# Optimization experiments

Measured on AMD Instinct MI355X. Metric: run time of the kernel, lower is better.

The kernel has to match this reference:

```python
import jax, jax.numpy as jnp
import numpy as np

C = 256
NUM_HEADS = 8
GROUPS = 8
EPS = 1e-5


def setup_inputs() -> dict:
    key = jax.random.key(0)
    ks = jax.random.split(key, 7)
    B, H, W = 2, 64, 64
    x = jax.random.normal(ks[0], (B, C, H, W), dtype=jnp.float32)
    gn_weight = jnp.ones((C,), dtype=jnp.float32)
    gn_bias = jnp.zeros((C,), dtype=jnp.float32)
    # 1x1 convs == per-pixel linear layers
    w_qkv = jax.random.normal(ks[1], (3 * C, C), dtype=jnp.float32) * (1.0 / np.sqrt(C))
    b_qkv = jax.random.normal(ks[2], (3 * C,), dtype=jnp.float32) * 0.01
    w_proj = jax.random.normal(ks[3], (C, C), dtype=jnp.float32) * (1.0 / np.sqrt(C))
    b_proj = jax.random.normal(ks[4], (C,), dtype=jnp.float32) * 0.01
    return {"x": x, "gn_weight": gn_weight, "gn_bias": gn_bias,
            "w_qkv": w_qkv, "b_qkv": b_qkv, "w_proj": w_proj, "b_proj": b_proj}


def reference(x, gn_weight, gn_bias, w_qkv, b_qkv, w_proj, b_proj):
    B, Cc, H, W = x.shape
    nh = NUM_HEADS
    hd = Cc // nh
    N = H * W
    scale = hd ** (-0.5)

    # GroupNorm(8, C): normalize over (C/G, H, W) per group, biased variance
    xg = x.reshape(B, GROUPS, Cc // GROUPS, H, W)
    mean = xg.mean(axis=(2, 3, 4), keepdims=True)
    var = xg.var(axis=(2, 3, 4), keepdims=True)
    hn = (xg - mean) * jax.lax.rsqrt(var + EPS)
    hn = hn.reshape(B, Cc, H, W) * gn_weight[None, :, None, None] + gn_bias[None, :, None, None]

    hf = hn.reshape(B, Cc, N)                       # [B, C, N]
    qkv = jnp.einsum('oc,bcn->bon', w_qkv, hf) + b_qkv[None, :, None]  # [B, 3C, N]
    qkv = qkv.reshape(B, 3, nh, hd, N)
    # q,k,v: [B, nh, N, hd]
    q = jnp.transpose(qkv[:, 0], (0, 1, 3, 2))
    k = jnp.transpose(qkv[:, 1], (0, 1, 3, 2))
    v = jnp.transpose(qkv[:, 2], (0, 1, 3, 2))

    attn = jnp.einsum('bhqd,bhkd->bhqk', q, k) * scale  # [B, nh, N, N]
    attn = jax.nn.softmax(attn, axis=-1)
    o = jnp.einsum('bhqk,bhkd->bhqd', attn, v)           # [B, nh, N, hd]
    o = jnp.transpose(o, (0, 1, 3, 2)).reshape(B, Cc, H, W)

    of = o.reshape(B, Cc, N)
    out = jnp.einsum('oc,bcn->bon', w_proj, of) + b_proj[None, :, None]
    return out.reshape(B, Cc, H, W)
```

## Files before the change

### kernel.cpp

```cpp
#include <hip/hip_runtime.h>


typedef _Float16 half8 __attribute__((ext_vector_type(8)));
typedef __fp16   fp16x2 __attribute__((ext_vector_type(2)));
typedef float    f32x4 __attribute__((ext_vector_type(4)));
typedef int      int2v __attribute__((ext_vector_type(2)));
typedef int      int4v __attribute__((ext_vector_type(4)));

__device__ __forceinline__ f32x4 mfma16(half8 a, half8 b, f32x4 c) {
  return __builtin_amdgcn_mfma_f32_16x16x32_f16(a, b, c, 0, 0, 0);
}

#if __has_builtin(__builtin_amdgcn_exp2f)
#define EXP2(x) __builtin_amdgcn_exp2f(x)
#else
#define EXP2(x) exp2f(x)
#endif

__device__ __forceinline__ unsigned short h_bits(_Float16 h) {
  return __builtin_bit_cast(unsigned short, h);
}
__device__ __forceinline__ int h2_bits(fp16x2 h) {
  return __builtin_bit_cast(int, h);
}

constexpr float CSCALE = (float)(1.4426950408889634 / 5.656854249492381);

__global__ __launch_bounds__(256) void gn_stats(const float* __restrict__ x,
                                                float* __restrict__ stats) {
  const int bg = blockIdx.x, ch = blockIdx.y, tid = threadIdx.x;
  const float* p = x + (size_t)bg * 131072 + (size_t)ch * 4096;
  float s = 0.f, ss = 0.f;
#pragma unroll
  for (int j = 0; j < 4; ++j) {
    f32x4 v = *(const f32x4*)(p + j * 1024 + tid * 4);
#pragma unroll
    for (int k = 0; k < 4; ++k) { s += v[k]; ss += v[k] * v[k]; }
  }
#pragma unroll
  for (int m = 1; m <= 32; m <<= 1) { s += __shfl_xor(s, m); ss += __shfl_xor(ss, m); }
  __shared__ float red[8];
  const int wv = tid >> 6;
  if ((tid & 63) == 0) { red[wv * 2] = s; red[wv * 2 + 1] = ss; }
  __syncthreads();
  if (tid == 0) {
    float S = red[0] + red[2] + red[4] + red[6];
    float SS = red[1] + red[3] + red[5] + red[7];
    atomicAdd(&stats[bg * 2], S);
    atomicAdd(&stats[bg * 2 + 1], SS);
  }
}

__global__ __launch_bounds__(256) void gn_apply(const float* __restrict__ x,
                                                const float* __restrict__ gw,
                                                const float* __restrict__ gb,
                                                const float* __restrict__ stats,
                                                _Float16* __restrict__ hn) {
  __shared__ float tile[64 * 65];
  const int tid = threadIdx.x;
  const int a = tid & 15;
  const int row16 = tid >> 4;
  const int b = blockIdx.z, c0 = blockIdx.y * 64, n0 = blockIdx.x * 64;
#pragma unroll
  for (int m = 0; m < 4; ++m) {
    const int cl = row16 + 16 * m;
    const int c = c0 + cl;
    const int g = c >> 5;
    const float s = stats[(b * 8 + g) * 2];
    const float ss = stats[(b * 8 + g) * 2 + 1];
    const float mean = s * (1.f / 131072.f);
    const float var = ss * (1.f / 131072.f) - mean * mean;
    const float rstd = rsqrtf(var + 1e-5f);
    const float ga = gw[c] * rstd;
    const float be = gb[c] - mean * ga;
    f32x4 xv = *(const f32x4*)(x + ((size_t)(b * 256 + c)) * 4096 + n0 + a * 4);
#pragma unroll
    for (int j = 0; j < 4; ++j) tile[cl * 65 + a * 4 + j] = xv[j] * ga + be;
  }
  __syncthreads();
#pragma unroll
  for (int m = 0; m < 4; ++m) {
    const int nl = row16 + 16 * m;
    const int cb = a * 4;
    int2v uh;
    unsigned short hh[4];
#pragma unroll
    for (int j = 0; j < 4; ++j) {
      hh[j] = h_bits((_Float16)tile[(cb + j) * 65 + nl]);
    }
    uh[0] = hh[0] | (hh[1] << 16); uh[1] = hh[2] | (hh[3] << 16);
    size_t off = ((size_t)(b * 4096 + n0 + nl)) * 256 + c0 + cb;
    *(int2v*)(hn + off) = uh;
  }
}

__global__ __launch_bounds__(256) void wcast(const float* __restrict__ wq,
                                             const float* __restrict__ wp,
                                             _Float16* __restrict__ wqh,
                                             _Float16* __restrict__ wph) {
  const int idx = blockIdx.x * 256 + threadIdx.x;
  if (idx < 196608) {
    wqh[idx] = (_Float16)wq[idx];
  } else {
    wph[idx - 196608] = (_Float16)wp[idx - 196608];
  }
}

template <int MODE>
__global__ __launch_bounds__(256) void gemm_f16(
    const _Float16* __restrict__ W, const _Float16* __restrict__ Bm,
    const float* __restrict__ bias,
    _Float16* __restrict__ qkT, _Float16* __restrict__ v_t,
    float* __restrict__ outp) {
  __shared__ _Float16 a_lds[2][4096];
  __shared__ _Float16 b_lds[2][4096];
  const int tid = threadIdx.x, lane = tid & 63, wv = tid >> 6;
  const int qq = lane >> 4, ii = lane & 15;
  const int m0 = blockIdx.x * 64, n0 = blockIdx.y * 64, bz = blockIdx.z;

  const _Float16* asrc[2];
  const _Float16* bsrc[2];
  int dst8[2];
#pragma unroll
  for (int rep = 0; rep < 2; ++rep) {
    const int idx = tid + 256 * rep;
    dst8[rep] = idx * 8;
    const int j = idx >> 7, c = (idx >> 6) & 1, l = idx & 63;
    const int lq = l >> 4, li = l & 15;
    asrc[rep] = W + (size_t)(m0 + 16 * j + li) * 256 + 32 * c + 8 * lq;
    bsrc[rep] = Bm + ((size_t)(bz * 4096 + n0 + 16 * j + li)) * 256 + 32 * c + 8 * lq;
  }

  f32x4 acc[4] = {};

  half8 ar0 = *(const half8*)asrc[0];
  half8 ar1 = *(const half8*)asrc[1];
  half8 br0 = *(const half8*)bsrc[0];
  half8 br1 = *(const half8*)bsrc[1];
  *(half8*)(a_lds[0] + dst8[0]) = ar0;
  *(half8*)(a_lds[0] + dst8[1]) = ar1;
  *(half8*)(b_lds[0] + dst8[0]) = br0;
  *(half8*)(b_lds[0] + dst8[1]) = br1;
  __syncthreads();

  for (int it = 0; it < 4; ++it) {
    const int cur = it & 1;
    if (it < 3) {
      const int ko = (it + 1) * 64;
      ar0 = *(const half8*)(asrc[0] + ko);
      ar1 = *(const half8*)(asrc[1] + ko);
      br0 = *(const half8*)(bsrc[0] + ko);
      br1 = *(const half8*)(bsrc[1] + ko);
    }
    half8 ah0 = *(const half8*)(a_lds[cur] + ((wv * 2 + 0) * 64 + lane) * 8);
    half8 ah1 = *(const half8*)(a_lds[cur] + ((wv * 2 + 1) * 64 + lane) * 8);
#pragma unroll
    for (int t = 0; t < 4; ++t) {
      half8 b0 = *(const half8*)(b_lds[cur] + ((t * 2 + 0) * 64 + lane) * 8);
      half8 b1 = *(const half8*)(b_lds[cur] + ((t * 2 + 1) * 64 + lane) * 8);
      acc[t] = mfma16(ah0, b0, acc[t]);
      acc[t] = mfma16(ah1, b1, acc[t]);
    }
    if (it < 3) {
      _Float16* an = a_lds[cur ^ 1];
      _Float16* bn = b_lds[cur ^ 1];
      *(half8*)(an + dst8[0]) = ar0;
      *(half8*)(an + dst8[1]) = ar1;
      *(half8*)(bn + dst8[0]) = br0;
      *(half8*)(bn + dst8[1]) = br1;
    }
    __syncthreads();
  }

  const int och0 = m0 + 16 * wv + 4 * qq;
  if (MODE == 0) {
    if (m0 < 512) {
      const float sc = (m0 < 256) ? CSCALE : 1.0f;
#pragma unroll
      for (int t = 0; t < 4; ++t) {
        const int n = n0 + 16 * t + ii;
        unsigned short hh[4];
#pragma unroll
        for (int r = 0; r < 4; ++r) {
          hh[r] = h_bits((_Float16)((acc[t][r] + bias[och0 + r]) * sc));
        }
        int2v u;
        u[0] = hh[0] | (hh[1] << 16);
        u[1] = hh[2] | (hh[3] << 16);
        *(int2v*)(qkT + ((size_t)(bz * 4096 + n)) * 512 + och0) = u;
      }
    } else {
#pragma unroll
      for (int t = 0; t < 4; ++t) {
#pragma unroll
        for (int r = 0; r < 4; ++r) {
          const int och = och0 + r;
          const int d = och - 512;
          const int hd_ = d & 31, head = d >> 5;
          const int n = n0 + 16 * t + ii;
          v_t[((size_t)((bz * 8 + head) * 32 + hd_)) * 4096 + n] =
              (_Float16)(acc[t][r] + bias[och]);
        }
      }
    }
  } else {
#pragma unroll
    for (int t = 0; t < 4; ++t) {
#pragma unroll
      for (int r = 0; r < 4; ++r) {
        const int och = och0 + r;
        const int n = n0 + 16 * t + ii;
        outp[((size_t)(bz * 256 + och)) * 4096 + n] = acc[t][r] + bias[och];
      }
    }
  }
}

__global__ __launch_bounds__(256) void attn_kernel(
    const _Float16* __restrict__ qkT, const _Float16* __restrict__ v_t,
    float* __restrict__ opart, float* __restrict__ lpart) {
  __shared__ _Float16 k_lds[2][4096];
  __shared__ _Float16 v_lds[2][4096];
  const int tid = threadIdx.x, lane = tid & 63, wv = tid >> 6;
  const int qq = lane >> 4, ii = lane & 15;
  const int bh = blockIdx.y, b = bh >> 3, h = bh & 7;
  const int n0 = blockIdx.x * 128;
  const int part = blockIdx.z;
  const int key0 = part * 2048;

  const _Float16* qbase =
      qkT + ((size_t)(b * 4096 + n0 + 32 * wv + ii)) * 512 + h * 32 + 8 * qq;
  half8 qf0 = *(const half8*)qbase;
  half8 qf1 = *(const half8*)(qbase + (size_t)16 * 512);

  const _Float16* ksrc[2];
  const _Float16* vsrc[2];
  int dst8[2];
#pragma unroll
  for (int rep = 0; rep < 2; ++rep) {
    const int idx = tid + 256 * rep;
    dst8[rep] = idx * 8;
    const int f = idx >> 6, l = idx & 63;
    const int fq = l >> 4, fi = l & 15;
    const int u = f >> 1, hf = f & 1;
    const int g = 32 * u + 4 * hf + 8 * (fi >> 2) + (fi & 3);
    ksrc[rep] = qkT + ((size_t)(b * 4096 + key0 + g)) * 512 + 256 + h * 32 + 8 * fq;
    vsrc[rep] = v_t + ((size_t)(bh * 32 + 16 * hf + fi)) * 4096 + key0 + 32 * u + 8 * fq;
  }

  half8 ones8;
#pragma unroll
  for (int j = 0; j < 8; ++j) ones8[j] = (_Float16)1.0f;

  f32x4 o00 = {}, o10 = {}, o01 = {}, o11 = {}, accl0 = {}, accl1 = {};

  half8 kr0 = *(const half8*)ksrc[0];
  half8 kr1 = *(const half8*)ksrc[1];
  half8 vr0 = *(const half8*)vsrc[0];
  half8 vr1 = *(const half8*)vsrc[1];
  *(half8*)(k_lds[0] + dst8[0]) = kr0;
  *(half8*)(k_lds[0] + dst8[1]) = kr1;
  *(half8*)(v_lds[0] + dst8[0]) = vr0;
  *(half8*)(v_lds[0] + dst8[1]) = vr1;
  __syncthreads();

  for (int kb = 0; kb < 16; ++kb) {
    const int cur = kb & 1;
    if (kb < 15) {
      const size_t ko = (size_t)(kb + 1) * 128 * 512;
      const size_t vo = (size_t)(kb + 1) * 128;
      kr0 = *(const half8*)(ksrc[0] + ko);
      kr1 = *(const half8*)(ksrc[1] + ko);
      vr0 = *(const half8*)(vsrc[0] + vo);
      vr1 = *(const half8*)(vsrc[1] + vo);
    }
    const _Float16* kbase = k_lds[cur];
    const _Float16* vbase = v_lds[cur];

#pragma unroll
    for (int u = 0; u < 4; ++u) {
      half8 kfa = *(const half8*)(kbase + u * 1024 + lane * 8);
      half8 kfb = *(const half8*)(kbase + u * 1024 + 512 + lane * 8);
      f32x4 z = {};
      f32x4 sa0 = mfma16(kfa, qf0, z);
      f32x4 sb0 = mfma16(kfb, qf0, z);
      f32x4 sa1 = mfma16(kfa, qf1, z);
      f32x4 sb1 = mfma16(kfb, qf1, z);
      int4v p0, p1;
      p0[0] = h2_bits(__builtin_amdgcn_cvt_pkrtz(EXP2(sa0[0]), EXP2(sa0[1])));
      p0[1] = h2_bits(__builtin_amdgcn_cvt_pkrtz(EXP2(sa0[2]), EXP2(sa0[3])));
      p0[2] = h2_bits(__builtin_amdgcn_cvt_pkrtz(EXP2(sb0[0]), EXP2(sb0[1])));
      p0[3] = h2_bits(__builtin_amdgcn_cvt_pkrtz(EXP2(sb0[2]), EXP2(sb0[3])));
      p1[0] = h2_bits(__builtin_amdgcn_cvt_pkrtz(EXP2(sa1[0]), EXP2(sa1[1])));
      p1[1] = h2_bits(__builtin_amdgcn_cvt_pkrtz(EXP2(sa1[2]), EXP2(sa1[3])));
      p1[2] = h2_bits(__builtin_amdgcn_cvt_pkrtz(EXP2(sb1[0]), EXP2(sb1[1])));
      p1[3] = h2_bits(__builtin_amdgcn_cvt_pkrtz(EXP2(sb1[2]), EXP2(sb1[3])));
      half8 pt0 = __builtin_bit_cast(half8, p0);
      half8 pt1 = __builtin_bit_cast(half8, p1);
      half8 vf0 = *(const half8*)(vbase + u * 1024 + lane * 8);
      half8 vf1 = *(const half8*)(vbase + u * 1024 + 512 + lane * 8);
      o00 = mfma16(vf0, pt0, o00);
      o10 = mfma16(vf1, pt0, o10);
      accl0 = mfma16(ones8, pt0, accl0);
      o01 = mfma16(vf0, pt1, o01);
      o11 = mfma16(vf1, pt1, o11);
      accl1 = mfma16(ones8, pt1, accl1);
    }

    if (kb < 15) {
      _Float16* kn = k_lds[cur ^ 1];
      _Float16* vn = v_lds[cur ^ 1];
      *(half8*)(kn + dst8[0]) = kr0;
      *(half8*)(kn + dst8[1]) = kr1;
      *(half8*)(vn + dst8[0]) = vr0;
      *(half8*)(vn + dst8[1]) = vr1;
    }
    __syncthreads();
  }

#pragma unroll
  for (int hf = 0; hf < 2; ++hf) {
    const f32x4 oa = hf ? o01 : o00;
    const f32x4 ob = hf ? o11 : o10;
    const int q = n0 + 32 * wv + 16 * hf + ii;
    float* base = opart + ((size_t)((part * 2 + b) * 4096 + q)) * 256 + h * 32;
    *(f32x4*)(base + 4 * qq) = oa;
    *(f32x4*)(base + 16 + 4 * qq) = ob;
    if (qq == 0) {
      lpart[((size_t)((part * 2 + b) * 4096 + q)) * 8 + h] = hf ? accl1[0] : accl0[0];
    }
  }
}

__global__ __launch_bounds__(256) void attn_combine(
    const float* __restrict__ opart, const float* __restrict__ lpart,
    _Float16* __restrict__ o16) {
  const int c = threadIdx.x, hh = c >> 5;
#pragma unroll
  for (int k = 0; k < 4; ++k) {
    const int row = blockIdx.x * 4 + k;
    const int b = row >> 12;
    const size_t i0 = ((size_t)(0 * 2 + b) * 4096 + (row & 4095)) * 256 + c;
    const size_t i1 = ((size_t)(1 * 2 + b) * 4096 + (row & 4095)) * 256 + c;
    const size_t l0i = ((size_t)(0 * 2 + b) * 4096 + (row & 4095)) * 8 + hh;
    const size_t l1i = ((size_t)(1 * 2 + b) * 4096 + (row & 4095)) * 8 + hh;
    const float O = opart[i0] + opart[i1];
    const float inv = 1.0f / (lpart[l0i] + lpart[l1i]);
    o16[(size_t)row * 256 + c] = (_Float16)(O * inv);
  }
}

extern "C" void kernel_launch(void* const* d_in, const int* in_sizes, int n_in,
                              void* d_out, int out_size, void* d_ws, size_t ws_size,
                              hipStream_t stream) {
  const float* x     = (const float*)d_in[0];
  const float* gnw   = (const float*)d_in[1];
  const float* gnb   = (const float*)d_in[2];
  const float* wqkv  = (const float*)d_in[3];
  const float* bqkv  = (const float*)d_in[4];
  const float* wproj = (const float*)d_in[5];
  const float* bproj = (const float*)d_in[6];
  float* out = (float*)d_out;

  char* ws = (char*)d_ws;
  size_t off = 0;
  auto alloc = [&](size_t bytes) -> char* {
    char* p = ws + off;
    off += (bytes + 255) & ~(size_t)255;
    return p;
  };
  float*    stats  = (float*)alloc(128);
  _Float16* hn     = (_Float16*)alloc((size_t)2 * 4096 * 256 * 2);
  _Float16* wq_h   = (_Float16*)alloc((size_t)768 * 256 * 2);
  _Float16* wp_h   = (_Float16*)alloc((size_t)256 * 256 * 2);
  _Float16* qkT    = (_Float16*)alloc((size_t)2 * 4096 * 512 * 2);
  _Float16* v_t    = (_Float16*)alloc((size_t)16 * 32 * 4096 * 2);
  float*    opart  = (float*)alloc((size_t)4 * 4096 * 256 * 4);
  float*    lpart  = (float*)alloc((size_t)4 * 4096 * 8 * 4);
  _Float16* o16 = hn;
  if (off > ws_size) return;

  (void)hipMemsetAsync(stats, 0, 256, stream);
  gn_stats<<<dim3(16, 32), 256, 0, stream>>>(x, stats);
  gn_apply<<<dim3(64, 4, 2), 256, 0, stream>>>(x, gnw, gnb, stats, hn);
  wcast<<<1024, 256, 0, stream>>>(wqkv, wproj, wq_h, wp_h);
  gemm_f16<0><<<dim3(12, 64, 2), 256, 0, stream>>>(wq_h, hn, bqkv, qkT, v_t,
                                                   nullptr);
  attn_kernel<<<dim3(32, 16, 2), 256, 0, stream>>>(qkT, v_t, opart, lpart);
  attn_combine<<<2048, 256, 0, stream>>>(opart, lpart, o16);
  gemm_f16<1><<<dim3(4, 64, 2), 256, 0, stream>>>(wp_h, o16, bproj, nullptr,
                                                  nullptr, out);
}
```

Before: 163.3 us.

## Split attention keys into four partitions with smaller 64-key LDS tiles

The attention kernel now processes 64-key tiles instead of 128, halving LDS per block, and sets a launch-bounds occupancy hint of 8 blocks. It splits keys across four partitions (falling back to two if workspace is short), doubling grid size from 1024 to 2048 blocks for better CU fill. The combine kernel loops over a variable number of partitions. The trade-off is more partial-output traffic in fp32, a heavier combine pass, and twice as many barriers per key processed.

```diff
diff --git a/kernel.cpp b/kernel.cpp
--- a/kernel.cpp
+++ b/kernel.cpp
@@ -216,37 +216,32 @@
   }
 }
 
-__global__ __launch_bounds__(256) void attn_kernel(
+__global__ __launch_bounds__(256, 8) void attn_kernel(
     const _Float16* __restrict__ qkT, const _Float16* __restrict__ v_t,
-    float* __restrict__ opart, float* __restrict__ lpart) {
-  __shared__ _Float16 k_lds[2][4096];
-  __shared__ _Float16 v_lds[2][4096];
+    float* __restrict__ opart, float* __restrict__ lpart, int nkb) {
+  __shared__ _Float16 k_lds[2][2048];
+  __shared__ _Float16 v_lds[2][2048];
   const int tid = threadIdx.x, lane = tid & 63, wv = tid >> 6;
   const int qq = lane >> 4, ii = lane & 15;
   const int bh = blockIdx.y, b = bh >> 3, h = bh & 7;
   const int n0 = blockIdx.x * 128;
   const int part = blockIdx.z;
-  const int key0 = part * 2048;
+  const int key0 = part * (nkb * 64);
 
   const _Float16* qbase =
       qkT + ((size_t)(b * 4096 + n0 + 32 * wv + ii)) * 512 + h * 32 + 8 * qq;
   half8 qf0 = *(const half8*)qbase;
   half8 qf1 = *(const half8*)(qbase + (size_t)16 * 512);
 
-  const _Float16* ksrc[2];
-  const _Float16* vsrc[2];
-  int dst8[2];
-#pragma unroll
-  for (int rep = 0; rep < 2; ++rep) {
-    const int idx = tid + 256 * rep;
-    dst8[rep] = idx * 8;
-    const int f = idx >> 6, l = idx & 63;
-    const int fq = l >> 4, fi = l & 15;
-    const int u = f >> 1, hf = f & 1;
-    const int g = 32 * u + 4 * hf + 8 * (fi >> 2) + (fi & 3);
-    ksrc[rep] = qkT + ((size_t)(b * 4096 + key0 + g)) * 512 + 256 + h * 32 + 8 * fq;
-    vsrc[rep] = v_t + ((size_t)(bh * 32 + 16 * hf + fi)) * 4096 + key0 + 32 * u + 8 * fq;
-  }
+  const int dst8 = tid * 8;
+  const int f = tid >> 6, l = tid & 63;
+  const int fq = l >> 4, fi = l & 15;
+  const int su = f >> 1, shf = f & 1;
+  const int g = 32 * su + 4 * shf + 8 * (fi >> 2) + (fi & 3);
+  const _Float16* ksrc =
+      qkT + ((size_t)(b * 4096 + key0 + g)) * 512 + 256 + h * 32 + 8 * fq;
+  const _Float16* vsrc =
+      v_t + ((size_t)(bh * 32 + 16 * shf + fi)) * 4096 + key0 + 32 * su + 8 * fq;
 
   half8 ones8;
 #pragma unroll
@@ -254,31 +249,23 @@
 
   f32x4 o00 = {}, o10 = {}, o01 = {}, o11 = {}, accl0 = {}, accl1 = {};
 
-  half8 kr0 = *(const half8*)ksrc[0];
-  half8 kr1 = *(const half8*)ksrc[1];
-  half8 vr0 = *(const half8*)vsrc[0];
-  half8 vr1 = *(const half8*)vsrc[1];
-  *(half8*)(k_lds[0] + dst8[0]) = kr0;
-  *(half8*)(k_lds[0] + dst8[1]) = kr1;
-  *(half8*)(v_lds[0] + dst8[0]) = vr0;
-  *(half8*)(v_lds[0] + dst8[1]) = vr1;
+  half8 kr = *(const half8*)ksrc;
+  half8 vr = *(const half8*)vsrc;
+  *(half8*)(k_lds[0] + dst8) = kr;
+  *(half8*)(v_lds[0] + dst8) = vr;
   __syncthreads();
 
-  for (int kb = 0; kb < 16; ++kb) {
+  for (int kb = 0; kb < nkb; ++kb) {
     const int cur = kb & 1;
-    if (kb < 15) {
-      const size_t ko = (size_t)(kb + 1) * 128 * 512;
-      const size_t vo = (size_t)(kb + 1) * 128;
-      kr0 = *(const half8*)(ksrc[0] + ko);
-      kr1 = *(const half8*)(ksrc[1] + ko);
-      vr0 = *(const half8*)(vsrc[0] + vo);
-      vr1 = *(const half8*)(vsrc[1] + vo);
+    if (kb < nkb - 1) {
+      kr = *(const half8*)(ksrc + (size_t)(kb + 1) * (64 * 512));
+      vr = *(const half8*)(vsrc + (size_t)(kb + 1) * 64);
     }
     const _Float16* kbase = k_lds[cur];
     const _Float16* vbase = v_lds[cur];
 
 #pragma unroll
-    for (int u = 0; u < 4; ++u) {
+    for (int u = 0; u < 2; ++u) {
       half8 kfa = *(const half8*)(kbase + u * 1024 + lane * 8);
       half8 kfb = *(const half8*)(kbase + u * 1024 + 512 + lane * 8);
       f32x4 z = {};
@@ -307,13 +294,9 @@
       accl1 = mfma16(ones8, pt1, accl1);
     }
 
-    if (kb < 15) {
-      _Float16* kn = k_lds[cur ^ 1];
-      _Float16* vn = v_lds[cur ^ 1];
-      *(half8*)(kn + dst8[0]) = kr0;
-      *(half8*)(kn + dst8[1]) = kr1;
-      *(half8*)(vn + dst8[0]) = vr0;
-      *(half8*)(vn + dst8[1]) = vr1;
+    if (kb < nkb - 1) {
+      *(half8*)(k_lds[cur ^ 1] + dst8) = kr;
+      *(half8*)(v_lds[cur ^ 1] + dst8) = vr;
     }
     __syncthreads();
   }
@@ -334,18 +317,19 @@
 
 __global__ __launch_bounds__(256) void attn_combine(
     const float* __restrict__ opart, const float* __restrict__ lpart,
-    _Float16* __restrict__ o16) {
+    _Float16* __restrict__ o16, int parts) {
   const int c = threadIdx.x, hh = c >> 5;
 #pragma unroll
   for (int k = 0; k < 4; ++k) {
     const int row = blockIdx.x * 4 + k;
     const int b = row >> 12;
-    const size_t i0 = ((size_t)(0 * 2 + b) * 4096 + (row & 4095)) * 256 + c;
-    const size_t i1 = ((size_t)(1 * 2 + b) * 4096 + (row & 4095)) * 256 + c;
-    const size_t l0i = ((size_t)(0 * 2 + b) * 4096 + (row & 4095)) * 8 + hh;
-    const size_t l1i = ((size_t)(1 * 2 + b) * 4096 + (row & 4095)) * 8 + hh;
-    const float O = opart[i0] + opart[i1];
-    const float inv = 1.0f / (lpart[l0i] + lpart[l1i]);
+    const int q = row & 4095;
+    float O = 0.f, L = 0.f;
+    for (int p = 0; p < parts; ++p) {
+      O += opart[((size_t)((p * 2 + b) * 4096 + q)) * 256 + c];
+      L += lpart[((size_t)((p * 2 + b) * 4096 + q)) * 8 + hh];
+    }
+    const float inv = 1.0f / L;
     o16[(size_t)row * 256 + c] = (_Float16)(O * inv);
   }
 }
@@ -375,8 +359,14 @@
   _Float16* wp_h   = (_Float16*)alloc((size_t)256 * 256 * 2);
   _Float16* qkT    = (_Float16*)alloc((size_t)2 * 4096 * 512 * 2);
   _Float16* v_t    = (_Float16*)alloc((size_t)16 * 32 * 4096 * 2);
-  float*    opart  = (float*)alloc((size_t)4 * 4096 * 256 * 4);
-  float*    lpart  = (float*)alloc((size_t)4 * 4096 * 8 * 4);
+
+  int parts = 4;
+  {
+    const size_t need4 = (size_t)8 * 4096 * 256 * 4 + (size_t)8 * 4096 * 8 * 4 + 1024;
+    if (off + need4 > ws_size) parts = 2;
+  }
+  float*    opart  = (float*)alloc((size_t)(parts * 2) * 4096 * 256 * 4);
+  float*    lpart  = (float*)alloc((size_t)(parts * 2) * 4096 * 8 * 4);
   _Float16* o16 = hn;
   if (off > ws_size) return;
 
@@ -386,8 +376,10 @@
   wcast<<<1024, 256, 0, stream>>>(wqkv, wproj, wq_h, wp_h);
   gemm_f16<0><<<dim3(12, 64, 2), 256, 0, stream>>>(wq_h, hn, bqkv, qkT, v_t,
                                                    nullptr);
-  attn_kernel<<<dim3(32, 16, 2), 256, 0, stream>>>(qkT, v_t, opart, lpart);
-  attn_combine<<<2048, 256, 0, stream>>>(opart, lpart, o16);
+  const int nkb = 64 / parts;
+  attn_kernel<<<dim3(32, 16, parts), 256, 0, stream>>>(qkT, v_t, opart, lpart,
+                                                       nkb);
+  attn_combine<<<2048, 256, 0, stream>>>(opart, lpart, o16, parts);
   gemm_f16<1><<<dim3(4, 64, 2), 256, 0, stream>>>(wp_h, o16, bproj, nullptr,
                                                   nullptr, out);
 }
```

New measurement: 224.5 us. 1.37x slower.
